# Kernel tuning notes

Hardware: AMD Instinct MI355X
Metric: run time of the kernel (lower is better)

Reference implementation:

```python
import jax, jax.numpy as jnp
import numpy as np

D_MODEL = 256
NUM_HEADS = 8
DIM_HEAD = D_MODEL // NUM_HEADS
EPS = 1e-6
MASK_BIAS = -1.0e9


def setup_inputs() -> dict:
    key = jax.random.key(0)
    ks = jax.random.split(key, 10)
    B, S = 2, 4096
    x = jax.random.normal(ks[0], (B, S, D_MODEL), dtype=jnp.float32)
    pad_mask = jnp.zeros((B, S), dtype=jnp.float32)  # 1.0 => padded position
    scale = 1.0 / np.sqrt(D_MODEL)
    Wq = jax.random.normal(ks[1], (D_MODEL, D_MODEL), dtype=jnp.float32) * scale
    bq = jnp.zeros((D_MODEL,), dtype=jnp.float32)
    Wk = jax.random.normal(ks[2], (D_MODEL, D_MODEL), dtype=jnp.float32) * scale
    bk = jnp.zeros((D_MODEL,), dtype=jnp.float32)
    Wv = jax.random.normal(ks[3], (D_MODEL, D_MODEL), dtype=jnp.float32) * scale
    bv = jnp.zeros((D_MODEL,), dtype=jnp.float32)
    gamma = jnp.ones((D_MODEL,), dtype=jnp.float32)
    beta = jnp.zeros((D_MODEL,), dtype=jnp.float32)
    return {"x": x, "pad_mask": pad_mask, "Wq": Wq, "bq": bq, "Wk": Wk,
            "bk": bk, "Wv": Wv, "bv": bv, "gamma": gamma, "beta": beta}


def _layer_norm(h, gamma, beta):
    mu = jnp.mean(h, axis=-1, keepdims=True)
    var = jnp.mean(jnp.square(h - mu), axis=-1, keepdims=True)
    return gamma * (h - mu) * jax.lax.rsqrt(var + EPS) + beta


def reference(x, pad_mask, Wq, bq, Wk, bk, Wv, bv, gamma, beta):
    B, S, D = x.shape
    q = x @ Wq + bq  # [B,S,D]
    k = x @ Wk + bk
    v = x @ Wv + bv
    # split heads: [B,S,D] -> [B,H,S,Dh]
    def split(t):
        return t.reshape(B, S, NUM_HEADS, DIM_HEAD).transpose(0, 2, 1, 3)
    qh, kh, vh = split(q), split(k), split(v)
    w = jnp.einsum("bhqd,bhkd->bhqk", qh, kh)  # [B,H,S,S]
    # faithful to source: mask added BEFORE the 1/sqrt(dim_head) scaling
    w = w + pad_mask[:, None, None, :] * MASK_BIAS
    w = w / jnp.sqrt(jnp.float32(DIM_HEAD))
    attn = jax.nn.softmax(w, axis=-1)
    # dropout is identity at inference
    out = jnp.einsum("bhqk,bhkd->bhqd", attn, vh)  # [B,H,S,Dh]
    out = out.transpose(0, 2, 1, 3).reshape(B, S, D)
    return _layer_norm(out + x, gamma, beta)
```

## Files before the change

### kernel.cpp

```cpp
#include <hip/hip_runtime.h>
#include <hip/hip_bf16.h>

#define D_MODEL 256
#define NUM_HEADS 8
#define DIM_HEAD 32
#define SEQ 4096
#define BATCH 2
#define NROWS (BATCH * SEQ)
#define LN_EPS 1e-6f
#define MASK_BIAS -1.0e9f
#define SCALE 0.17677669529663687f
#define LOG2E 1.4426950408889634f

typedef __attribute__((ext_vector_type(8))) short short8;
typedef __attribute__((ext_vector_type(4))) float f32x4;

static __device__ __forceinline__ unsigned short f2b(float f) {
    union { __hip_bfloat16 b; unsigned short u; } cv;
    cv.b = __float2bfloat16(f);
    return cv.u;
}
static __device__ __forceinline__ unsigned int pk_bf16(float lo, float hi) {
    union { __hip_bfloat162 v; unsigned int u; } cv;
    cv.v = __float22bfloat162_rn(make_float2(lo, hi));
    return cv.u;
}
static __device__ __forceinline__ float exp2_raw(float x) {
#if __has_builtin(__builtin_amdgcn_exp2f)
    return __builtin_amdgcn_exp2f(x);
#else
    float r;
    asm volatile("v_exp_f32 %0, %1" : "=v"(r) : "v"(x));
    return r;
#endif
}
static __device__ __forceinline__ void load_lds16(const void* g, void* l) {
    __builtin_amdgcn_global_load_lds(
        (const __attribute__((address_space(1))) unsigned int*)g,
        (__attribute__((address_space(3))) unsigned int*)l, 16, 0, 0);
}

__global__ __launch_bounds__(256) void prep_kernel(
    const float* __restrict__ Wq, const float* __restrict__ Wk,
    const float* __restrict__ Wv,
    const float* __restrict__ bq, const float* __restrict__ bk,
    const float* __restrict__ bv,
    const float* __restrict__ pad,
    unsigned short* __restrict__ Wt, float* __restrict__ biasc,
    float* __restrict__ T2)
{
    const int blk = blockIdx.x;
    const int t = threadIdx.x;
    if (blk < 768) {
        const int w = blk >> 8;
        const int k = blk & 255;
        const float* W = (w == 0) ? Wq : (w == 1) ? Wk : Wv;
        Wt[(size_t)(w * 256 + t) * 256 + k] = f2b(W[(size_t)k * 256 + t]);
        if (k == 0) {
            const float* bb = (w == 0) ? bq : (w == 1) ? bk : bv;
            biasc[w * 256 + t] = bb[t];
        }
    } else {
        const int i = (blk - 768) * 256 + t;
        T2[i] = pad[i] * (MASK_BIAS * SCALE * LOG2E);
    }
}

__global__ __launch_bounds__(256) void qkv_mfma_kernel(
    const float* __restrict__ x, const unsigned short* __restrict__ Wt,
    const float* __restrict__ biasc,
    unsigned short* __restrict__ Qh, unsigned short* __restrict__ Kh,
    unsigned short* __restrict__ Vt)
{
    const int lane = threadIdx.x & 63;
    const int wid  = threadIdx.x >> 6;
    const int c    = lane & 15;
    const int quad = lane >> 4;

    const int rb = blockIdx.x / 12;
    const int cb = blockIdx.x % 12;
    const int r0 = rb * 64 + wid * 16;
    const int n0 = cb * 64;
    const bool isV = (n0 >= 512);

    f32x4 acc[4];
    #pragma unroll
    for (int t = 0; t < 4; t++) acc[t] = (f32x4){0.f, 0.f, 0.f, 0.f};

    const float* xp0 = x + (size_t)(r0 + c) * D_MODEL + quad * 8;
    const unsigned short* wp0 = Wt + (size_t)(n0 + c) * 256 + quad * 8;

    if (!isV) {
        for (int k0 = 0; k0 < 256; k0 += 32) {
            const float4 a0 = *(const float4*)(xp0 + k0);
            const float4 a1 = *(const float4*)(xp0 + k0 + 4);
            union { unsigned int u[4]; short8 s; } af;
            af.u[0] = pk_bf16(a0.x, a0.y);
            af.u[1] = pk_bf16(a0.z, a0.w);
            af.u[2] = pk_bf16(a1.x, a1.y);
            af.u[3] = pk_bf16(a1.z, a1.w);
            #pragma unroll
            for (int t = 0; t < 4; t++) {
                const short8 bf = *(const short8*)(wp0 + (size_t)(16 * t) * 256 + k0);
                acc[t] = __builtin_amdgcn_mfma_f32_16x16x32_bf16(bf, af.s, acc[t], 0, 0, 0);
            }
        }
        const int row = r0 + c;
        const int bb = row >> 12;
        const int s  = row & (SEQ - 1);
        unsigned short* base = (n0 < 256) ? Qh : Kh;
        #pragma unroll
        for (int t = 0; t < 4; t++) {
            const int dim = (n0 & 255) + 16 * t + quad * 4;
            const int h = dim >> 5, d = dim & 31;
            const float4 b4 = *(const float4*)(biasc + n0 + 16 * t + quad * 4);
            const size_t bh = (size_t)(bb * NUM_HEADS + h);
            uint2 pk = make_uint2(pk_bf16(acc[t][0] + b4.x, acc[t][1] + b4.y),
                                  pk_bf16(acc[t][2] + b4.z, acc[t][3] + b4.w));
            *(uint2*)(base + (bh * SEQ + s) * DIM_HEAD + d) = pk;
        }
    } else {
        for (int k0 = 0; k0 < 256; k0 += 32) {
            const float4 a0 = *(const float4*)(xp0 + k0);
            const float4 a1 = *(const float4*)(xp0 + k0 + 4);
            union { unsigned int u[4]; short8 s; } af;
            af.u[0] = pk_bf16(a0.x, a0.y);
            af.u[1] = pk_bf16(a0.z, a0.w);
            af.u[2] = pk_bf16(a1.x, a1.y);
            af.u[3] = pk_bf16(a1.z, a1.w);
            #pragma unroll
            for (int t = 0; t < 4; t++) {
                const short8 bf = *(const short8*)(wp0 + (size_t)(16 * t) * 256 + k0);
                acc[t] = __builtin_amdgcn_mfma_f32_16x16x32_bf16(af.s, bf, acc[t], 0, 0, 0);
            }
        }
        const int row = r0 + quad * 4;
        const int bb = row >> 12;
        const int s  = row & (SEQ - 1);
        #pragma unroll
        for (int t = 0; t < 4; t++) {
            const int dim = (n0 & 255) + 16 * t + c;
            const int h = dim >> 5, d = dim & 31;
            const float bv = biasc[n0 + 16 * t + c];
            const size_t bh = (size_t)(bb * NUM_HEADS + h);
            uint2 pk = make_uint2(pk_bf16(acc[t][0] + bv, acc[t][1] + bv),
                                  pk_bf16(acc[t][2] + bv, acc[t][3] + bv));
            *(uint2*)(Vt + (bh * DIM_HEAD + d) * SEQ + s) = pk;
        }
    }
}

__global__ __launch_bounds__(256, 8) void attn_mfma_kernel(
    const unsigned short* __restrict__ Qh, const unsigned short* __restrict__ Kh,
    const unsigned short* __restrict__ Vt, const float* __restrict__ T2,
    float* __restrict__ P1, float* __restrict__ P2,
    float* __restrict__ L1, float* __restrict__ L2)
{
    __shared__ __align__(16) unsigned short ldsK[2][64 * 32];
    __shared__ __align__(16) unsigned short ldsV[2][32 * 64];
    __shared__ __align__(16) float          ldsT[2][64];

    const int lane = threadIdx.x & 63;
    const int wid  = threadIdx.x >> 6;
    const int c    = lane & 15;
    const int quad = lane >> 4;

    const int gw = blockIdx.x;
    const int e  = gw & 1;
    const int q0 = ((gw >> 1) & 63) * 64;
    const int h  = (gw >> 7) & (NUM_HEADS - 1);
    const int b  = gw >> 10;
    const size_t bh = (size_t)(b * NUM_HEADS + h);

    const float k2 = SCALE * LOG2E;
    const int perm = ((c & 12) << 1) | (c & 3);

    const unsigned short* Kb = Kh + bh * SEQ * DIM_HEAD;
    const unsigned short* Vb = Vt + bh * DIM_HEAD * SEQ;
    const float* Tb = T2 + (size_t)b * SEQ;
    const int sbase = e * (SEQ / 2);

    const int qrow = q0 + wid * 16;
    const short8 qf = *(const short8*)(Qh + (bh * SEQ + qrow + c) * DIM_HEAD + quad * 8);

    union { unsigned int u[4]; short8 s; } ones;
    ones.u[0] = ones.u[1] = ones.u[2] = ones.u[3] = 0x3F803F80u;

    const int f0 = ((perm >> 1) ^ (perm >> 3)) & 3;
    const int f1 = (((perm + 4) >> 1) ^ ((perm + 4) >> 3)) & 3;
    const int kA = perm * 32 + ((quad ^ f0) << 3);
    const int kB = (perm + 4) * 32 + ((quad ^ f1) << 3);
    const int g0 = quad ^ (c & 7);
    const int vA0 = c * 64 + (g0 << 3);
    const int vA1 = c * 64 + ((g0 ^ 4) << 3);
    const int vB0 = (16 + c) * 64 + (g0 << 3);
    const int vB1 = (16 + c) * 64 + ((g0 ^ 4) << 3);

    const int skey = (lane >> 2);
    const int sgK  = lane & 3;
    const int sdim = lane >> 3;
    const int sgV  = lane & 7;

    f32x4 o0 = {0.f,0.f,0.f,0.f}, o1 = {0.f,0.f,0.f,0.f};
    f32x4 lacc = {0.f,0.f,0.f,0.f};
    const f32x4 z = {0.f, 0.f, 0.f, 0.f};

    auto stage = [&](int lch, int pb) {
        const int s0 = sbase + lch * 64;
        if (wid < 2) {
            #pragma unroll
            for (int jj = 0; jj < 2; jj++) {
                const int j = wid * 2 + jj;
                const int key = j * 16 + skey;
                const int f = ((key >> 1) ^ (key >> 3)) & 3;
                load_lds16(Kb + (size_t)(s0 + key) * 32 + ((sgK ^ f) << 3),
                           &ldsK[pb][j * 512]);
            }
        } else {
            #pragma unroll
            for (int jj = 0; jj < 2; jj++) {
                const int j = (wid - 2) * 2 + jj;
                const int dim = j * 8 + sdim;
                load_lds16(Vb + (size_t)dim * SEQ + s0 + ((sgV ^ (dim & 7)) << 3),
                           &ldsV[pb][j * 512]);
            }
            if (wid == 3 && lane < 16)
                load_lds16(Tb + s0 + lane * 4, &ldsT[pb][0]);
        }
    };

    auto sub = [&](int pb, int s) {
        const short8 kf0 = *(const short8*)&ldsK[pb][s * 1024 + kA];
        const short8 kf1 = *(const short8*)&ldsK[pb][s * 1024 + kB];
        const short8 vf0 = *(const short8*)&ldsV[pb][s ? vA1 : vA0];
        const short8 vf1 = *(const short8*)&ldsV[pb][s ? vB1 : vB0];
        const float4 t0 = *(const float4*)&ldsT[pb][s * 32 + quad * 8];
        const float4 t1 = *(const float4*)&ldsT[pb][s * 32 + quad * 8 + 4];

        const f32x4 st0 = __builtin_amdgcn_mfma_f32_16x16x32_bf16(kf0, qf, z, 0, 0, 0);
        const f32x4 st1 = __builtin_amdgcn_mfma_f32_16x16x32_bf16(kf1, qf, z, 0, 0, 0);

        float p[8];
        p[0] = exp2_raw(fmaf(st0[0], k2, t0.x));
        p[1] = exp2_raw(fmaf(st0[1], k2, t0.y));
        p[2] = exp2_raw(fmaf(st0[2], k2, t0.z));
        p[3] = exp2_raw(fmaf(st0[3], k2, t0.w));
        p[4] = exp2_raw(fmaf(st1[0], k2, t1.x));
        p[5] = exp2_raw(fmaf(st1[1], k2, t1.y));
        p[6] = exp2_raw(fmaf(st1[2], k2, t1.z));
        p[7] = exp2_raw(fmaf(st1[3], k2, t1.w));

        union { unsigned int u[4]; short8 s8; } pf;
        pf.u[0] = pk_bf16(p[0], p[1]);
        pf.u[1] = pk_bf16(p[2], p[3]);
        pf.u[2] = pk_bf16(p[4], p[5]);
        pf.u[3] = pk_bf16(p[6], p[7]);

        lacc = __builtin_amdgcn_mfma_f32_16x16x32_bf16(ones.s, pf.s8, lacc, 0, 0, 0);
        o0   = __builtin_amdgcn_mfma_f32_16x16x32_bf16(vf0,   pf.s8, o0,   0, 0, 0);
        o1   = __builtin_amdgcn_mfma_f32_16x16x32_bf16(vf1,   pf.s8, o1,   0, 0, 0);
    };

    stage(0, 0);
    __syncthreads();
    for (int ch = 0; ch < 32; ++ch) {
        const int pb = ch & 1;
        stage((ch + 1) & 31, pb ^ 1);
        sub(pb, 0);
        sub(pb, 1);
        __syncthreads();
    }

    float* Pe = e ? P2 : P1;
    float* op = Pe + ((size_t)(b * SEQ) + qrow + c) * D_MODEL + h * DIM_HEAD + quad * 4;
    *(float4*)op        = make_float4(o0[0], o0[1], o0[2], o0[3]);
    *(float4*)(op + 16) = make_float4(o1[0], o1[1], o1[2], o1[3]);
    if (quad == 0) {
        float* Le = e ? L2 : L1;
        Le[((size_t)(b * SEQ) + qrow + c) * NUM_HEADS + h] = lacc[0];
    }
}

__global__ __launch_bounds__(256) void ln_kernel(
    float* P1,
    const float* __restrict__ P2,
    const float* __restrict__ L1, const float* __restrict__ L2,
    const float* __restrict__ x,
    const float* __restrict__ gamma, const float* __restrict__ beta)
{
    const int lane = threadIdx.x & 63;
    const int wid  = threadIdx.x >> 6;
    const size_t row = (size_t)blockIdx.x * 4 + wid;
    const int h = lane >> 3;

    const float4 a  = ((const float4*)(P1 + row * D_MODEL))[lane];
    const float4 p2 = ((const float4*)(P2 + row * D_MODEL))[lane];
    const float4 xv = ((const float4*)(x + row * D_MODEL))[lane];
    const float inv = 1.0f / (L1[row * NUM_HEADS + h] + L2[row * NUM_HEADS + h]);

    float hv[4];
    hv[0] = (a.x + p2.x) * inv + xv.x;
    hv[1] = (a.y + p2.y) * inv + xv.y;
    hv[2] = (a.z + p2.z) * inv + xv.z;
    hv[3] = (a.w + p2.w) * inv + xv.w;

    float s = hv[0] + hv[1] + hv[2] + hv[3];
    #pragma unroll
    for (int off = 32; off > 0; off >>= 1) s += __shfl_xor(s, off, 64);
    const float mu = s * (1.0f / D_MODEL);

    float d0 = hv[0]-mu, d1 = hv[1]-mu, d2 = hv[2]-mu, d3 = hv[3]-mu;
    float ss = d0*d0 + d1*d1 + d2*d2 + d3*d3;
    #pragma unroll
    for (int off = 32; off > 0; off >>= 1) ss += __shfl_xor(ss, off, 64);
    const float rs = rsqrtf(ss * (1.0f / D_MODEL) + LN_EPS);

    const float4 g  = ((const float4*)gamma)[lane];
    const float4 bb = ((const float4*)beta)[lane];
    float4 y;
    y.x = g.x * d0 * rs + bb.x;
    y.y = g.y * d1 * rs + bb.y;
    y.z = g.z * d2 * rs + bb.z;
    y.w = g.w * d3 * rs + bb.w;
    ((float4*)(P1 + row * D_MODEL))[lane] = y;
}

extern "C" void kernel_launch(void* const* d_in, const int* in_sizes, int n_in,
                              void* d_out, int out_size, void* d_ws, size_t ws_size,
                              hipStream_t stream)
{
    const float* x     = (const float*)d_in[0];
    const float* pad   = (const float*)d_in[1];
    const float* Wq    = (const float*)d_in[2];
    const float* bq    = (const float*)d_in[3];
    const float* Wk    = (const float*)d_in[4];
    const float* bk    = (const float*)d_in[5];
    const float* Wv    = (const float*)d_in[6];
    const float* bv    = (const float*)d_in[7];
    const float* gamma = (const float*)d_in[8];
    const float* beta  = (const float*)d_in[9];

    const size_t elems = (size_t)NROWS * D_MODEL;
    unsigned short* Qh = (unsigned short*)d_ws;
    unsigned short* Kh = Qh + elems;
    unsigned short* Vt = Kh + elems;
    float* T2 = (float*)(Vt + elems);
    unsigned short* Wt = (unsigned short*)(T2 + NROWS);
    float* biasc = (float*)(Wt + 768 * 256);
    float* P2 = biasc + 768;
    float* L1 = P2 + elems;
    float* L2 = L1 + (size_t)NROWS * NUM_HEADS;
    float* P1 = (float*)d_out;

    prep_kernel<<<800, 256, 0, stream>>>(Wq, Wk, Wv, bq, bk, bv, pad,
                                         Wt, biasc, T2);
    qkv_mfma_kernel<<<(NROWS / 64) * 12, 256, 0, stream>>>(x, Wt, biasc,
                                                           Qh, Kh, Vt);
    attn_mfma_kernel<<<BATCH * NUM_HEADS * (SEQ / 64) * 2, 256, 0, stream>>>(
        Qh, Kh, Vt, T2, P1, P2, L1, L2);
    ln_kernel<<<NROWS / 4, 256, 0, stream>>>(P1, P2, L1, L2, x, gamma, beta);
}
```

Baseline: 198.7 us.

## Pre-convert x to bf16 once and precompute attention staging pointers

The prep kernel gains 1024 extra blocks that convert x to a bf16 copy once. The QKV GEMM then reads that copy directly instead of loading fp32 and converting it in each of the 12 column blocks, which halves the x traffic in the GEMM and removes repeated conversions. The attention kernel now computes its K/V/T global staging pointers once and advances them each chunk, with the loop unrolled by 2, to cut per-iteration address arithmetic. The trade-off is an extra full write and read of x in the prep kernel plus more workspace.

```diff
diff --git a/kernel.cpp b/kernel.cpp
--- a/kernel.cpp
+++ b/kernel.cpp
@@ -45,9 +45,9 @@
     const float* __restrict__ Wv,
     const float* __restrict__ bq, const float* __restrict__ bk,
     const float* __restrict__ bv,
-    const float* __restrict__ pad,
+    const float* __restrict__ pad, const float* __restrict__ x,
     unsigned short* __restrict__ Wt, float* __restrict__ biasc,
-    float* __restrict__ T2)
+    float* __restrict__ T2, unsigned short* __restrict__ xc)
 {
     const int blk = blockIdx.x;
     const int t = threadIdx.x;
@@ -60,14 +60,24 @@
             const float* bb = (w == 0) ? bq : (w == 1) ? bk : bv;
             biasc[w * 256 + t] = bb[t];
         }
-    } else {
+    } else if (blk < 800) {
         const int i = (blk - 768) * 256 + t;
         T2[i] = pad[i] * (MASK_BIAS * SCALE * LOG2E);
+    } else {
+        const size_t i8 = (size_t)(blk - 800) * 256 + t;
+        const float4 a0 = ((const float4*)x)[i8 * 2];
+        const float4 a1 = ((const float4*)x)[i8 * 2 + 1];
+        uint4 o;
+        o.x = pk_bf16(a0.x, a0.y);
+        o.y = pk_bf16(a0.z, a0.w);
+        o.z = pk_bf16(a1.x, a1.y);
+        o.w = pk_bf16(a1.z, a1.w);
+        ((uint4*)xc)[i8] = o;
     }
 }
 
 __global__ __launch_bounds__(256) void qkv_mfma_kernel(
-    const float* __restrict__ x, const unsigned short* __restrict__ Wt,
+    const unsigned short* __restrict__ xc, const unsigned short* __restrict__ Wt,
     const float* __restrict__ biasc,
     unsigned short* __restrict__ Qh, unsigned short* __restrict__ Kh,
     unsigned short* __restrict__ Vt)
@@ -87,22 +97,16 @@
     #pragma unroll
     for (int t = 0; t < 4; t++) acc[t] = (f32x4){0.f, 0.f, 0.f, 0.f};
 
-    const float* xp0 = x + (size_t)(r0 + c) * D_MODEL + quad * 8;
+    const unsigned short* xp0 = xc + (size_t)(r0 + c) * D_MODEL + quad * 8;
     const unsigned short* wp0 = Wt + (size_t)(n0 + c) * 256 + quad * 8;
 
     if (!isV) {
         for (int k0 = 0; k0 < 256; k0 += 32) {
-            const float4 a0 = *(const float4*)(xp0 + k0);
-            const float4 a1 = *(const float4*)(xp0 + k0 + 4);
-            union { unsigned int u[4]; short8 s; } af;
-            af.u[0] = pk_bf16(a0.x, a0.y);
-            af.u[1] = pk_bf16(a0.z, a0.w);
-            af.u[2] = pk_bf16(a1.x, a1.y);
-            af.u[3] = pk_bf16(a1.z, a1.w);
+            const short8 af = *(const short8*)(xp0 + k0);
             #pragma unroll
             for (int t = 0; t < 4; t++) {
                 const short8 bf = *(const short8*)(wp0 + (size_t)(16 * t) * 256 + k0);
-                acc[t] = __builtin_amdgcn_mfma_f32_16x16x32_bf16(bf, af.s, acc[t], 0, 0, 0);
+                acc[t] = __builtin_amdgcn_mfma_f32_16x16x32_bf16(bf, af, acc[t], 0, 0, 0);
             }
         }
         const int row = r0 + c;
@@ -121,17 +125,11 @@
         }
     } else {
         for (int k0 = 0; k0 < 256; k0 += 32) {
-            const float4 a0 = *(const float4*)(xp0 + k0);
-            const float4 a1 = *(const float4*)(xp0 + k0 + 4);
-            union { unsigned int u[4]; short8 s; } af;
-            af.u[0] = pk_bf16(a0.x, a0.y);
-            af.u[1] = pk_bf16(a0.z, a0.w);
-            af.u[2] = pk_bf16(a1.x, a1.y);
-            af.u[3] = pk_bf16(a1.z, a1.w);
+            const short8 af = *(const short8*)(xp0 + k0);
             #pragma unroll
             for (int t = 0; t < 4; t++) {
                 const short8 bf = *(const short8*)(wp0 + (size_t)(16 * t) * 256 + k0);
-                acc[t] = __builtin_amdgcn_mfma_f32_16x16x32_bf16(af.s, bf, acc[t], 0, 0, 0);
+                acc[t] = __builtin_amdgcn_mfma_f32_16x16x32_bf16(af, bf, acc[t], 0, 0, 0);
             }
         }
         const int row = r0 + quad * 4;
@@ -190,42 +188,52 @@
     const int f1 = (((perm + 4) >> 1) ^ ((perm + 4) >> 3)) & 3;
     const int kA = perm * 32 + ((quad ^ f0) << 3);
     const int kB = (perm + 4) * 32 + ((quad ^ f1) << 3);
-    const int g0 = quad ^ (c & 7);
-    const int vA0 = c * 64 + (g0 << 3);
-    const int vA1 = c * 64 + ((g0 ^ 4) << 3);
-    const int vB0 = (16 + c) * 64 + (g0 << 3);
-    const int vB1 = (16 + c) * 64 + ((g0 ^ 4) << 3);
-
-    const int skey = (lane >> 2);
-    const int sgK  = lane & 3;
-    const int sdim = lane >> 3;
-    const int sgV  = lane & 7;
+    const int g0i = quad ^ (c & 7);
+    const int vA0 = c * 64 + (g0i << 3);
+    const int vA1 = c * 64 + ((g0i ^ 4) << 3);
+    const int vB0 = (16 + c) * 64 + (g0i << 3);
+    const int vB1 = (16 + c) * 64 + ((g0i ^ 4) << 3);
+
+    const unsigned short *gp0, *gp1;
+    const float* gT = Tb + sbase + lane * 4;
+    int d0ofs, d1ofs;
+    if (wid < 2) {
+        const int skey = lane >> 2, sgK = lane & 3;
+        const int key0 = (wid * 2)     * 16 + skey;
+        const int key1 = (wid * 2 + 1) * 16 + skey;
+        const int fa = ((key0 >> 1) ^ (key0 >> 3)) & 3;
+        const int fb = ((key1 >> 1) ^ (key1 >> 3)) & 3;
+        gp0 = Kb + (size_t)(sbase + key0) * 32 + ((sgK ^ fa) << 3);
+        gp1 = Kb + (size_t)(sbase + key1) * 32 + ((sgK ^ fb) << 3);
+        d0ofs = (wid * 2) * 512;
+        d1ofs = (wid * 2 + 1) * 512;
+    } else {
+        const int sdim = lane >> 3, sgV = lane & 7;
+        const int dim0 = ((wid - 2) * 2)     * 8 + sdim;
+        const int dim1 = ((wid - 2) * 2 + 1) * 8 + sdim;
+        gp0 = Vb + (size_t)dim0 * SEQ + sbase + ((sgV ^ (dim0 & 7)) << 3);
+        gp1 = Vb + (size_t)dim1 * SEQ + sbase + ((sgV ^ (dim1 & 7)) << 3);
+        d0ofs = ((wid - 2) * 2) * 512;
+        d1ofs = ((wid - 2) * 2 + 1) * 512;
+    }
 
     f32x4 o0 = {0.f,0.f,0.f,0.f}, o1 = {0.f,0.f,0.f,0.f};
     f32x4 lacc = {0.f,0.f,0.f,0.f};
     const f32x4 z = {0.f, 0.f, 0.f, 0.f};
 
-    auto stage = [&](int lch, int pb) {
-        const int s0 = sbase + lch * 64;
+    auto stage = [&](int pb) {
         if (wid < 2) {
-            #pragma unroll
-            for (int jj = 0; jj < 2; jj++) {
-                const int j = wid * 2 + jj;
-                const int key = j * 16 + skey;
-                const int f = ((key >> 1) ^ (key >> 3)) & 3;
-                load_lds16(Kb + (size_t)(s0 + key) * 32 + ((sgK ^ f) << 3),
-                           &ldsK[pb][j * 512]);
+            load_lds16(gp0, &ldsK[pb][d0ofs]);
+            load_lds16(gp1, &ldsK[pb][d1ofs]);
+            gp0 += 64 * 32; gp1 += 64 * 32;
+        } else {
+            load_lds16(gp0, &ldsV[pb][d0ofs]);
+            load_lds16(gp1, &ldsV[pb][d1ofs]);
+            gp0 += 64; gp1 += 64;
+            if (wid == 3) {
+                if (lane < 16) load_lds16(gT, &ldsT[pb][0]);
+                gT += 64;
             }
-        } else {
-            #pragma unroll
-            for (int jj = 0; jj < 2; jj++) {
-                const int j = (wid - 2) * 2 + jj;
-                const int dim = j * 8 + sdim;
-                load_lds16(Vb + (size_t)dim * SEQ + s0 + ((sgV ^ (dim & 7)) << 3),
-                           &ldsV[pb][j * 512]);
-            }
-            if (wid == 3 && lane < 16)
-                load_lds16(Tb + s0 + lane * 4, &ldsT[pb][0]);
         }
     };
 
@@ -261,11 +269,12 @@
         o1   = __builtin_amdgcn_mfma_f32_16x16x32_bf16(vf1,   pf.s8, o1,   0, 0, 0);
     };
 
-    stage(0, 0);
+    stage(0);
     __syncthreads();
+    #pragma unroll 2
     for (int ch = 0; ch < 32; ++ch) {
         const int pb = ch & 1;
-        stage((ch + 1) & 31, pb ^ 1);
+        stage(pb ^ 1);
         sub(pb, 0);
         sub(pb, 1);
         __syncthreads();
@@ -350,11 +359,12 @@
     float* P2 = biasc + 768;
     float* L1 = P2 + elems;
     float* L2 = L1 + (size_t)NROWS * NUM_HEADS;
+    unsigned short* xc = (unsigned short*)(L2 + (size_t)NROWS * NUM_HEADS);
     float* P1 = (float*)d_out;
 
-    prep_kernel<<<800, 256, 0, stream>>>(Wq, Wk, Wv, bq, bk, bv, pad,
-                                         Wt, biasc, T2);
-    qkv_mfma_kernel<<<(NROWS / 64) * 12, 256, 0, stream>>>(x, Wt, biasc,
+    prep_kernel<<<1824, 256, 0, stream>>>(Wq, Wk, Wv, bq, bk, bv, pad, x,
+                                          Wt, biasc, T2, xc);
+    qkv_mfma_kernel<<<(NROWS / 64) * 12, 256, 0, stream>>>(xc, Wt, biasc,
                                                            Qh, Kh, Vt);
     attn_mfma_kernel<<<BATCH * NUM_HEADS * (SEQ / 64) * 2, 256, 0, stream>>>(
         Qh, Kh, Vt, T2, P1, P2, L1, L2);
```

Measured after the change: 197.9 us. Within noise of the previous version (-0.4%).
